# Optimization experiments

Measured on AMD Instinct MI355X. Metric: run time of the kernel, lower is better.

Reference implementation:

```python
import jax, jax.numpy as jnp
import numpy as np

B, H, V, W = 64, 4, 128000, 200  # batch, heads, vocab, repetition window
N = B * H
NEG = jnp.float32(-1e30)


def setup_inputs() -> dict:
    key = jax.random.key(0)
    ks = jax.random.split(key, 6)
    logits = jax.random.normal(ks[0], (B, H, V), jnp.float32) * 4.0
    output_tokens = jax.random.randint(ks[1], (N, W), 0, V)  # pad value would be V
    temperatures = jax.random.uniform(ks[2], (N,), jnp.float32, 0.5, 1.5)
    top_ps = jax.random.uniform(ks[3], (N,), jnp.float32, 0.7, 1.0)
    top_ks = jax.random.randint(ks[4], (N,), 1, 1025).astype(jnp.int32)
    repetition_penalties = jax.random.uniform(ks[5], (N,), jnp.float32, 1.0, 1.3)
    return {
        "logits": logits,
        "output_tokens": output_tokens,
        "temperatures": temperatures,
        "top_ps": top_ps,
        "top_ks": top_ks,
        "repetition_penalties": repetition_penalties,
    }


def reference(logits, output_tokens, temperatures, top_ps, top_ks, repetition_penalties):
    b, h, v = logits.shape
    n = b * h
    lg = logits.reshape(n, v)

    # --- repetition penalty (bincount-based mask, pad id = v is dropped) ---
    rows = jnp.arange(n)[:, None]
    counts = jnp.zeros((n, v + 1), jnp.int32).at[rows, output_tokens].add(1)[:, :v]
    seen = counts > 0
    rp = jnp.where(seen, repetition_penalties[:, None], 1.0)
    lg = jnp.where(lg > 0, lg / rp, lg * rp)

    # --- temperature ---
    lg = lg / temperatures[:, None]

    # --- top-k / top-p (vLLM: ascending sort, mask, scatter back) ---
    idx = jnp.argsort(lg, axis=-1)                       # ascending
    ls = jnp.take_along_axis(lg, idx, axis=-1)
    kth = jnp.take_along_axis(ls, (v - top_ks.astype(jnp.int32))[:, None], axis=-1)
    ls = jnp.where(ls < kth, NEG, ls)                    # top-k mask
    ps = jax.nn.softmax(ls, axis=-1)
    csum = jnp.cumsum(ps, axis=-1)
    pmask = (csum <= 1.0 - top_ps[:, None]).at[:, -1].set(False)
    ls = jnp.where(pmask, NEG, ls)                       # top-p mask
    inv = jnp.argsort(idx, axis=-1)                      # scatter back
    lg = jnp.take_along_axis(ls, inv, axis=-1)

    # --- softmax + multinomial sample (categorical == multinomial(probs, 1)) ---
    probs = jax.nn.softmax(lg, axis=-1)
    ids = jax.random.categorical(jax.random.key(42), lg, axis=-1).reshape(b, h)
    return ids, probs
```

## Files before the change

kernel.cpp:

```cpp
#include <hip/hip_runtime.h>

#define V 128000
#define V4 (V / 4)
#define NCHUNK (V / 16)
#define NROWS 256
#define NSLICE 8
#define SL4 (V4 / NSLICE)
#define W 200
#define VW (V / 32)
#define CAP 4096
#define CAPS 2048
#define CAPM 8192
#define TINYF 1.17549435e-38f
#define HIDX(b) ((b) + ((b) >> 5))
#define HSZ 4224

#define WS_CMAX   0u
#define WS_BMAX   4104192u
#define WS_NEED   16777216u

typedef float vfloat4 __attribute__((ext_vector_type(4)));

__device__ __forceinline__ unsigned int fkey(float x) {
  unsigned int u = __float_as_uint(x);
  return (u & 0x80000000u) ? ~u : (u | 0x80000000u);
}
__device__ __forceinline__ float ikey(unsigned int k) {
  unsigned int u = (k & 0x80000000u) ? (k & 0x7FFFFFFFu) : ~k;
  return __uint_as_float(u);
}

__device__ __forceinline__ unsigned int tf_bits(unsigned int t) {
  const unsigned int k0 = 0u, k1 = 42u;
  const unsigned int ks2 = k0 ^ k1 ^ 0x1BD11BDAu;
  unsigned int x0 = 0u + k0, x1 = t + k1;
  const unsigned int ksArr[3] = {k0, k1, ks2};
  const int RA[4] = {13, 15, 26, 6};
  const int RB[4] = {17, 29, 16, 24};
#pragma unroll
  for (int i = 0; i < 5; ++i) {
#pragma unroll
    for (int j = 0; j < 4; ++j) {
      int r = (i & 1) ? RB[j] : RA[j];
      x0 += x1;
      x1 = (x1 << r) | (x1 >> (32 - r));
      x1 ^= x0;
    }
    x0 += ksArr[(i + 1) % 3];
    x1 += ksArr[(i + 2) % 3] + (unsigned int)(i + 1);
  }
  return x0 ^ x1;
}

__device__ __forceinline__ float xform(float x, bool seen, float rp, float irp,
                                        float itemp) {
  if (seen) x = (x > 0.0f) ? x * irp : x * rp;
  return x * itemp;
}

__device__ __forceinline__ void wave_suffix_select_p(const int* hist, int need,
                                                     int lane, int* out_b,
                                                     int* out_rem) {
  int sm = 0;
  const int bb = lane * 64;
  for (int i = 0; i < 64; ++i) sm += hist[HIDX(bb + i)];
  int sfx = sm;
#pragma unroll
  for (int d = 1; d < 64; d <<= 1) {
    int t = __shfl_down(sfx, d);
    if (lane + d < 64) sfx += t;
  }
  unsigned long long mk = __ballot(sfx >= need);
  const int cstar = 63 - __builtin_clzll(mk);
  const int aboveC = __shfl(sfx, cstar) - __shfl(sm, cstar);
  int h = hist[HIDX(cstar * 64 + lane)];
  int sfx2 = h;
#pragma unroll
  for (int d = 1; d < 64; d <<= 1) {
    int t = __shfl_down(sfx2, d);
    if (lane + d < 64) sfx2 += t;
  }
  unsigned long long mk2 = __ballot(aboveC + sfx2 >= need);
  const int boff = 63 - __builtin_clzll(mk2);
  const int aboveB = aboveC + __shfl(sfx2, boff) - __shfl(h, boff);
  if (lane == 0) {
    *out_b = cstar * 64 + boff;
    *out_rem = need - aboveB;
  }
}

__global__ __launch_bounds__(256) void kAZ_chunkmax(
    const float* __restrict__ logits, const int* __restrict__ toks,
    const float* __restrict__ temps, const float* __restrict__ rps,
    unsigned short* __restrict__ ws_cmax, float* __restrict__ ws_bmax,
    float* __restrict__ probs) {
  __shared__ unsigned int s_seen[VW];
  __shared__ float s_red[4];
  const int row = blockIdx.x >> 3;
  const int slice = blockIdx.x & 7;
  const int tid = threadIdx.x;
  const int lane = tid & 63;
  const int wid = tid >> 6;
  const float rp = rps[row];
  const float irp = 1.0f / rp;
  const float itemp = 1.0f / temps[row];
  const size_t base = (size_t)row * V;
  const float4* __restrict__ lg4 = reinterpret_cast<const float4*>(logits + base);
  vfloat4* __restrict__ pr4 = reinterpret_cast<vfloat4*>(probs + base);

  for (int i = tid; i < VW; i += 256) s_seen[i] = 0u;
  __syncthreads();
  for (int i = tid; i < W; i += 256) {
    int tok = toks[row * W + i];
    if (tok >= 0 && tok < V) atomicOr(&s_seen[tok >> 5], 1u << (tok & 31));
  }
  __syncthreads();

  float lmax = -INFINITY;
  const int q0 = slice * SL4;
  const vfloat4 z4 = (vfloat4){0.0f, 0.0f, 0.0f, 0.0f};
  for (int qi = tid; qi < SL4; qi += 256) {
    const int q = q0 + qi;
    float4 x4 = lg4[q];
    pr4[q] = z4;
    float xs[4] = {x4.x, x4.y, x4.z, x4.w};
    const int j0 = q * 4;
    const int sh = j0 & 31;
    unsigned long long ww = (unsigned long long)s_seen[j0 >> 5] |
                            ((unsigned long long)s_seen[(j0 + 3) >> 5] << 32);
    unsigned int kmax = 0u;
#pragma unroll
    for (int e = 0; e < 4; ++e) {
      float x = xform(xs[e], (ww >> (sh + e)) & 1ull, rp, irp, itemp);
      lmax = fmaxf(lmax, x);
      unsigned int ky = fkey(x);
      kmax = kmax > ky ? kmax : ky;
    }
    unsigned int o;
    o = __shfl_xor(kmax, 1); kmax = kmax > o ? kmax : o;
    o = __shfl_xor(kmax, 2); kmax = kmax > o ? kmax : o;
    if ((lane & 3) == 0) ws_cmax[row * NCHUNK + (q >> 2)] = (unsigned short)(kmax >> 16);
  }
#pragma unroll
  for (int d = 32; d > 0; d >>= 1) lmax = fmaxf(lmax, __shfl_xor(lmax, d));
  if (lane == 0) s_red[wid] = lmax;
  __syncthreads();
  if (tid == 0) {
    float mm = fmaxf(fmaxf(s_red[0], s_red[1]), fmaxf(s_red[2], s_red[3]));
    ws_bmax[row * NSLICE + slice] = mm;
  }
}

__global__ __launch_bounds__(1024) void kB_select(
    const float* __restrict__ logits, const int* __restrict__ toks,
    const float* __restrict__ temps, const float* __restrict__ topps,
    const int* __restrict__ topks, const float* __restrict__ rps,
    const unsigned short* __restrict__ ws_cmax, const float* __restrict__ ws_bmax,
    float* __restrict__ out_ids, float* __restrict__ probs) {
  __shared__ unsigned long long s_key[CAP];
  __shared__ __align__(16) unsigned char s_bufA[HSZ*4];
  __shared__ __align__(16) unsigned char s_bufB[16384];
  __shared__ __align__(16) float s_e2[CAPS];
  __shared__ __align__(16) float s_q2[CAPS];
  __shared__ unsigned char s_keep[CAPS];
  __shared__ float s_wredf[16];
  __shared__ int s_wredi[16];
  __shared__ float s_mv, s_dn1, s_dn2;
  __shared__ int s_b0, s_cnt, s_scnt, s_selb, s_selrem, s_p0v, s_maxpop;

  int* s_hist0 = (int*)s_key;
  unsigned int* s_seen = (unsigned int*)s_bufA;
  int* s_hist = (int*)s_bufA;
  unsigned short* s_cmax16 = (unsigned short*)s_bufB;
  unsigned long long* s_key2 = (unsigned long long*)s_bufB;
  unsigned long long* s_skey = s_key;

  const int row = blockIdx.x;
  const int tid = threadIdx.x;
  const int lane = tid & 63;
  const int wid = tid >> 6;
  const float rp = rps[row];
  const float irp = 1.0f / rp;
  const float itemp = 1.0f / temps[row];
  const float topp = topps[row];
  const int k = topks[row];
  const size_t base = (size_t)row * V;
  const float4* __restrict__ lg4 = reinterpret_cast<const float4*>(logits + base);
  float* __restrict__ prow = probs + base;

  for (int i = tid; i < VW; i += 1024) s_seen[i] = 0u;
  for (int i = tid; i < HSZ; i += 1024) s_hist0[i] = 0;
  {
    const unsigned int* cm32 = reinterpret_cast<const unsigned int*>(ws_cmax + row * NCHUNK);
    unsigned int* sc32 = reinterpret_cast<unsigned int*>(s_cmax16);
    for (int i = tid; i < NCHUNK / 2; i += 1024) sc32[i] = cm32[i];
  }
  __syncthreads();
  for (int i = tid; i < W; i += 1024) {
    int tok = toks[row * W + i];
    if (tok >= 0 && tok < V) atomicOr(&s_seen[tok >> 5], 1u << (tok & 31));
  }
  for (int i = tid; i < NCHUNK; i += 1024)
    atomicAdd(&s_hist0[HIDX(s_cmax16[i] >> 4)], 1);
  __syncthreads();

  if (wid == 1 && lane == 0) {
    float mm = ws_bmax[row * NSLICE];
    for (int i = 1; i < NSLICE; ++i) mm = fmaxf(mm, ws_bmax[row * NSLICE + i]);
    s_mv = mm;
  }
  if (wid == 0) {
    wave_suffix_select_p(s_hist0, k, lane, &s_b0, &s_selrem);
    if (lane == 0) s_cnt = 0;
  }
  __syncthreads();
  const int b0 = s_b0;

  const unsigned int fk0 = ((unsigned int)b0) << 20;
  const int c16 = b0 << 4;
  for (int qb = 0; qb < V4; qb += 1024) {
    const int q = qb + tid;
    const bool act = (q < V4) && ((int)s_cmax16[q >> 2] >= c16);
    unsigned int ks[4];
    bool pr[4] = {false, false, false, false};
    const int j0 = q * 4;
    if (act) {
      float4 x4 = lg4[q];
      float raw[4] = {x4.x, x4.y, x4.z, x4.w};
      const int sh = j0 & 31;
      unsigned long long ww = (unsigned long long)s_seen[j0 >> 5] |
                              ((unsigned long long)s_seen[(j0 + 3) >> 5] << 32);
#pragma unroll
      for (int e = 0; e < 4; ++e) {
        float x = xform(raw[e], (ww >> (sh + e)) & 1ull, rp, irp, itemp);
        ks[e] = fkey(x);
        pr[e] = (ks[e] >= fk0);
      }
    }
    int cnt = (int)pr[0] + (int)pr[1] + (int)pr[2] + (int)pr[3];
    int inc = cnt;
#pragma unroll
    for (int d = 1; d < 64; d <<= 1) {
      int t = __shfl_up(inc, d);
      if (lane >= d) inc += t;
    }
    const int total = __shfl(inc, 63);
    if (total) {
      int basep = 0;
      if (lane == 0) basep = atomicAdd(&s_cnt, total);
      basep = __shfl(basep, 0);
      int off = basep + inc - cnt;
#pragma unroll
      for (int e = 0; e < 4; ++e) {
        if (pr[e]) {
          if (off < CAP)
            s_key[off] = ((unsigned long long)ks[e] << 32) | (unsigned int)(j0 + e);
          ++off;
        }
      }
    }
  }
  __syncthreads();
  int G = s_cnt;
  if (G > CAP) G = CAP;
  const int kk = k > G ? G : k;

  for (int i = tid; i < HSZ; i += 1024) s_hist[i] = 0;
  __syncthreads();
  for (int i = tid; i < G; i += 1024)
    atomicAdd(&s_hist[HIDX((unsigned int)(s_key[i] >> 52))], 1);
  __syncthreads();
  if (wid == 0) {
    wave_suffix_select_p(s_hist, kk, lane, &s_selb, &s_selrem);
    if (lane == 0) s_scnt = 0;
  }
  __syncthreads();
  const unsigned int b1 = (unsigned int)s_selb;

  for (int ib = 0; ib < G; ib += 1024) {
    const int i = ib + tid;
    const bool p = (i < G) && ((unsigned int)(s_key[i] >> 52) >= b1);
    unsigned long long mask = __ballot(p);
    if (!mask) continue;
    int basep = 0;
    if (lane == 0) basep = atomicAdd(&s_scnt, __popcll(mask));
    basep = __shfl(basep, 0);
    if (p) {
      int pos = basep + __popcll(mask & ((1ull << lane) - 1ull));
      if (pos < CAPS) s_key2[pos] = s_key[i];
    }
  }
  __syncthreads();
  int S = s_scnt;
  if (S > CAPS) S = CAPS;
  const float m = s_mv;

  const unsigned int cbase = b1 << 20;
  const unsigned int span = fkey(m) - cbase;
  int shiftb;
  {
    int bits = 32 - __clz((int)(span | 1u));
    shiftb = bits > 12 ? bits - 12 : 0;
  }
  for (int i = tid; i < HSZ; i += 1024) s_hist[i] = 0;
  __syncthreads();
  for (int i = tid; i < S; i += 1024) {
    unsigned int hi = (unsigned int)(s_key2[i] >> 32);
    int b = (int)((hi - cbase) >> shiftb);
    if (b > 4095) b = 4095;
    atomicAdd(&s_hist[HIDX(b)], 1);
  }
  __syncthreads();
  if (wid == 0) {
    int T = 0, mx = 0;
    const int bb = lane * 64;
    for (int i = 0; i < 64; ++i) {
      int c = s_hist[HIDX(bb + i)];
      T += c;
      mx = c > mx ? c : mx;
    }
    int ex = T;
#pragma unroll
    for (int d = 1; d < 64; d <<= 1) {
      int t = __shfl_up(ex, d);
      if (lane >= d) ex += t;
    }
    ex -= T;
    int run = ex;
    for (int i = 0; i < 64; ++i) {
      int idx = HIDX(bb + i);
      int c = s_hist[idx];
      s_hist[idx] = run;
      run += c;
    }
#pragma unroll
    for (int d = 32; d > 0; d >>= 1) {
      int o = __shfl_xor(mx, d);
      mx = o > mx ? o : mx;
    }
    if (lane == 0) s_maxpop = mx;
  }
  __syncthreads();

  if (s_maxpop <= 16) {
    for (int i = tid; i < S; i += 1024) {
      unsigned long long key = s_key2[i];
      unsigned int hi = (unsigned int)(key >> 32);
      int b = (int)((hi - cbase) >> shiftb);
      if (b > 4095) b = 4095;
      int pos = atomicAdd(&s_hist[HIDX(b)], 1);
      s_skey[pos] = key;
    }
    __syncthreads();
    for (int b = tid; b < 4096; b += 1024) {
      int endb = s_hist[HIDX(b)];
      int st = (b == 0) ? 0 : s_hist[HIDX(b - 1)];
      for (int i = st + 1; i < endb; ++i) {
        unsigned long long key = s_skey[i];
        int j = i - 1;
        while (j >= st && s_skey[j] > key) {
          s_skey[j + 1] = s_skey[j];
          --j;
        }
        s_skey[j + 1] = key;
      }
    }
    __syncthreads();
  } else {
    int np2 = 2;
    while (np2 < S) np2 <<= 1;
    for (int i = S + tid; i < np2; i += 1024) s_key2[i] = ~0ull;
    __syncthreads();
    for (int size = 2; size <= np2; size <<= 1) {
      for (int stride = size >> 1; stride > 0; stride >>= 1) {
        for (int t2 = tid; t2 < (np2 >> 1); t2 += 1024) {
          int pos = 2 * t2 - (t2 & (stride - 1));
          int qq = pos + stride;
          bool up = ((pos & size) == 0);
          unsigned long long a = s_key2[pos], b = s_key2[qq];
          if ((a > b) == up) { s_key2[pos] = b; s_key2[qq] = a; }
        }
        __syncthreads();
      }
    }
    for (int i = tid; i < S; i += 1024) s_skey[i] = s_key2[i];
    __syncthreads();
  }

  const unsigned int kthkey32 = (unsigned int)(s_skey[S - kk] >> 32);
  for (int i = tid; i < S; i += 1024) {
    unsigned int hi = (unsigned int)(s_skey[i] >> 32);
    if (hi >= kthkey32 && (i == 0 || (unsigned int)(s_skey[i - 1] >> 32) < kthkey32))
      s_p0v = i;
  }
  __syncthreads();
  const int p0 = s_p0v;
  const int L = S - p0;

  float part = 0.0f;
  for (int i = tid; i < L; i += 1024) {
    float x = ikey((unsigned int)(s_skey[p0 + i] >> 32));
    float e = expf(x - m);
    s_e2[i] = e;
    part += e;
  }
#pragma unroll
  for (int d = 32; d > 0; d >>= 1) part += __shfl_xor(part, d);
  if (lane == 0) s_wredf[wid] = part;
  __syncthreads();
  if (tid == 0) {
    float s = 0.0f;
    for (int i = 0; i < 16; ++i) s += s_wredf[i];
    s_dn1 = s;
  }
  __syncthreads();
  const float denom = s_dn1;

  for (int i = tid; i < L; i += 1024) s_q2[i] = s_e2[i] / denom;
  __syncthreads();

  if (tid == 0) {
    const float cut = 1.0f - topp;
    float cs = 0.0f;
    int i = 0;
    for (; i + 16 <= L; i += 16) {
      vfloat4 a = *(const vfloat4*)&s_q2[i];
      vfloat4 b = *(const vfloat4*)&s_q2[i + 4];
      vfloat4 c = *(const vfloat4*)&s_q2[i + 8];
      vfloat4 d = *(const vfloat4*)&s_q2[i + 12];
      unsigned int w0, w1, w2, w3;
      cs += a.x; w0  = (cs <= cut) ? 0u : 1u;
      cs += a.y; w0 |= ((cs <= cut) ? 0u : 1u) << 8;
      cs += a.z; w0 |= ((cs <= cut) ? 0u : 1u) << 16;
      cs += a.w; w0 |= ((cs <= cut) ? 0u : 1u) << 24;
      cs += b.x; w1  = (cs <= cut) ? 0u : 1u;
      cs += b.y; w1 |= ((cs <= cut) ? 0u : 1u) << 8;
      cs += b.z; w1 |= ((cs <= cut) ? 0u : 1u) << 16;
      cs += b.w; w1 |= ((cs <= cut) ? 0u : 1u) << 24;
      cs += c.x; w2  = (cs <= cut) ? 0u : 1u;
      cs += c.y; w2 |= ((cs <= cut) ? 0u : 1u) << 8;
      cs += c.z; w2 |= ((cs <= cut) ? 0u : 1u) << 16;
      cs += c.w; w2 |= ((cs <= cut) ? 0u : 1u) << 24;
      cs += d.x; w3  = (cs <= cut) ? 0u : 1u;
      cs += d.y; w3 |= ((cs <= cut) ? 0u : 1u) << 8;
      cs += d.z; w3 |= ((cs <= cut) ? 0u : 1u) << 16;
      cs += d.w; w3 |= ((cs <= cut) ? 0u : 1u) << 24;
      *(unsigned int*)&s_keep[i] = w0;
      *(unsigned int*)&s_keep[i + 4] = w1;
      *(unsigned int*)&s_keep[i + 8] = w2;
      *(unsigned int*)&s_keep[i + 12] = w3;
    }
    for (; i < L; ++i) {
      cs += s_q2[i];
      s_keep[i] = (cs <= cut) ? 0 : 1;
    }
    s_keep[L - 1] = 1;
  }
  __syncthreads();

  part = 0.0f;
  for (int i = tid; i < L; i += 1024)
    if (s_keep[i]) part += s_e2[i];
#pragma unroll
  for (int d = 32; d > 0; d >>= 1) part += __shfl_xor(part, d);
  if (lane == 0) s_wredf[wid] = part;
  __syncthreads();
  if (tid == 0) {
    float s = 0.0f;
    for (int i = 0; i < 16; ++i) s += s_wredf[i];
    s_dn2 = s;
  }
  __syncthreads();
  const float denom2 = s_dn2;

  for (int i = tid; i < L; i += 1024)
    s_e2[i] = s_keep[i] ? (s_e2[i] / denom2) : 0.0f;
  __syncthreads();

  float bs = -INFINITY;
  int bi = 0x7FFFFFFF;
  for (int i = tid; i < L; i += 1024) {
    if (!s_keep[i]) continue;
    unsigned long long kv = s_skey[p0 + i];
    int j = (int)(kv & 0xFFFFFFFFull);
    float x = ikey((unsigned int)(kv >> 32));
    unsigned int t = (unsigned int)(row * V) + (unsigned int)j;
    unsigned int bb = tf_bits(t);
    float u = __uint_as_float((bb >> 9) | 0x3f800000u) - 1.0f;
    if (u < TINYF) u = TINYF;
    float g = -logf(-logf(u));
    float sc = x + g;
    if (sc > bs || (sc == bs && j < bi)) { bs = sc; bi = j; }
  }

  for (int i = tid; i < L; i += 1024) {
    int j = (int)(s_skey[p0 + i] & 0xFFFFFFFFull);
    prow[j] = s_e2[i];
  }

#pragma unroll
  for (int d = 32; d > 0; d >>= 1) {
    float ov = __shfl_down(bs, d);
    int oi = __shfl_down(bi, d);
    if (ov > bs || (ov == bs && oi < bi)) { bs = ov; bi = oi; }
  }
  if (lane == 0) { s_wredf[wid] = bs; s_wredi[wid] = bi; }
  __syncthreads();
  if (tid == 0) {
    float bb = s_wredf[0];
    int bj = s_wredi[0];
    for (int i = 1; i < 16; ++i) {
      if (s_wredf[i] > bb || (s_wredf[i] == bb && s_wredi[i] < bj)) {
        bb = s_wredf[i];
        bj = s_wredi[i];
      }
    }
    out_ids[row] = (float)bj;
  }
}

__global__ __launch_bounds__(1024, 1) void sampler_mono(
    const float* __restrict__ logits, const int* __restrict__ toks,
    const float* __restrict__ temps, const float* __restrict__ topps,
    const int* __restrict__ topks, const float* __restrict__ rps,
    float* __restrict__ out_ids, float* __restrict__ probs) {
  __shared__ unsigned int s_seen[VW];
  __shared__ int s_hist[4096];
  __shared__ unsigned short s_cmax16[NCHUNK];
  __shared__ float s_sval[CAPM];
  __shared__ int s_sidx[CAPM];
  __shared__ float s_e[CAPM];
  __shared__ unsigned char s_keep[CAPM];
  __shared__ float s_wredf[16];
  __shared__ int s_wredi[16];
  __shared__ float s_m, s_denom, s_denom2;
  __shared__ int s_b0, s_cnt, s_p0;

  const int row = blockIdx.x;
  const int tid = threadIdx.x;
  const int lane = tid & 63;
  const int wid = tid >> 6;
  const float rp = rps[row];
  const float irp = 1.0f / rp;
  const float itemp = 1.0f / temps[row];
  const float topp = topps[row];
  const int k = topks[row];
  const size_t base = (size_t)row * V;
  const float4* __restrict__ lg4 = reinterpret_cast<const float4*>(logits + base);
  vfloat4* __restrict__ pr4 = reinterpret_cast<vfloat4*>(probs + base);

  for (int i = tid; i < VW; i += 1024) s_seen[i] = 0u;
  for (int i = tid; i < 4096; i += 1024) s_hist[i] = 0;
  __syncthreads();
  for (int i = tid; i < W; i += 1024) {
    int tok = toks[row * W + i];
    if (tok >= 0 && tok < V) atomicOr(&s_seen[tok >> 5], 1u << (tok & 31));
  }
  __syncthreads();

  float lmax = -INFINITY;
  for (int qb = 0; qb < V4; qb += 1024) {
    const int q = qb + tid;
    unsigned int kmax = 0u;
    if (q < V4) {
      float4 x4 = lg4[q];
      float xs[4] = {x4.x, x4.y, x4.z, x4.w};
      const int j0 = q * 4;
      const int sh = j0 & 31;
      unsigned long long ww = (unsigned long long)s_seen[j0 >> 5] |
                              ((unsigned long long)s_seen[(j0 + 3) >> 5] << 32);
#pragma unroll
      for (int e = 0; e < 4; ++e) {
        float x = xform(xs[e], (ww >> (sh + e)) & 1ull, rp, irp, itemp);
        lmax = fmaxf(lmax, x);
        unsigned int ky = fkey(x);
        kmax = kmax > ky ? kmax : ky;
      }
    }
    unsigned int o;
    o = __shfl_xor(kmax, 1); kmax = kmax > o ? kmax : o;
    o = __shfl_xor(kmax, 2); kmax = kmax > o ? kmax : o;
    if (((lane & 3) == 0) && (q < V4)) s_cmax16[q >> 2] = (unsigned short)(kmax >> 16);
  }
#pragma unroll
  for (int d = 32; d > 0; d >>= 1) lmax = fmaxf(lmax, __shfl_xor(lmax, d));
  if (lane == 0) s_wredf[wid] = lmax;
  __syncthreads();
  for (int i = tid; i < NCHUNK; i += 1024)
    atomicAdd(&s_hist[s_cmax16[i] >> 4], 1);
  __syncthreads();
  if (wid == 1 && lane == 0) {
    float mm = s_wredf[0];
    for (int i = 1; i < 16; ++i) mm = fmaxf(mm, s_wredf[i]);
    s_m = mm;
  }
  if (wid == 0) {
    int sm = 0;
    const int bb = lane * 64;
    for (int i = 0; i < 64; ++i) sm += s_hist[bb + i];
    int sfx = sm;
#pragma unroll
    for (int d = 1; d < 64; d <<= 1) {
      int t = __shfl_down(sfx, d);
      if (lane + d < 64) sfx += t;
    }
    unsigned long long mk = __ballot(sfx >= k);
    const int cstar = 63 - __builtin_clzll(mk);
    const int above = __shfl(sfx, cstar) - __shfl(sm, cstar);
    int h = s_hist[cstar * 64 + lane];
    int sfx2 = h;
#pragma unroll
    for (int d = 1; d < 64; d <<= 1) {
      int t = __shfl_down(sfx2, d);
      if (lane + d < 64) sfx2 += t;
    }
    unsigned long long mk2 = __ballot(above + sfx2 >= k);
    const int boff = 63 - __builtin_clzll(mk2);
    if (lane == 0) { s_b0 = cstar * 64 + boff; s_cnt = 0; }
  }
  __syncthreads();
  const int b0 = s_b0;
  const unsigned int fk0 = ((unsigned int)b0) << 20;
  const int c16 = b0 << 4;
  for (int qb = 0; qb < V4; qb += 1024) {
    const int q = qb + tid;
    const bool act = (q < V4) && ((int)s_cmax16[q >> 2] >= c16);
    float xs[4];
    bool pr[4] = {false, false, false, false};
    const int j0 = q * 4;
    if (act) {
      float4 x4 = lg4[q];
      float raw[4] = {x4.x, x4.y, x4.z, x4.w};
      const int sh = j0 & 31;
      unsigned long long ww = (unsigned long long)s_seen[j0 >> 5] |
                              ((unsigned long long)s_seen[(j0 + 3) >> 5] << 32);
#pragma unroll
      for (int e = 0; e < 4; ++e) {
        xs[e] = xform(raw[e], (ww >> (sh + e)) & 1ull, rp, irp, itemp);
        pr[e] = (fkey(xs[e]) >= fk0);
      }
    }
#pragma unroll
    for (int e = 0; e < 4; ++e) {
      unsigned long long mask = __ballot(pr[e]);
      if (!mask) continue;
      int basep = 0;
      if (lane == 0) basep = atomicAdd(&s_cnt, __popcll(mask));
      basep = __shfl(basep, 0);
      if (pr[e]) {
        int pos = basep + __popcll(mask & ((1ull << lane) - 1ull));
        if (pos < CAPM) { s_sval[pos] = xs[e]; s_sidx[pos] = j0 + e; }
      }
    }
  }
  __syncthreads();
  int G = s_cnt;
  if (G > CAPM) G = CAPM;
  int np2 = 2;
  while (np2 < G) np2 <<= 1;
  for (int i = G + tid; i < np2; i += 1024) {
    s_sval[i] = INFINITY;
    s_sidx[i] = 0x7FFFFFFF;
  }
  __syncthreads();
  for (int size = 2; size <= np2; size <<= 1) {
    for (int stride = size >> 1; stride > 0; stride >>= 1) {
      for (int t2 = tid; t2 < (np2 >> 1); t2 += 1024) {
        int pos = 2 * t2 - (t2 & (stride - 1));
        int qq = pos + stride;
        bool up = ((pos & size) == 0);
        float v1 = s_sval[pos], v2 = s_sval[qq];
        int i1 = s_sidx[pos], i2 = s_sidx[qq];
        bool gt = (v1 > v2) || (v1 == v2 && i1 > i2);
        if (gt == up) {
          s_sval[pos] = v2; s_sval[qq] = v1;
          s_sidx[pos] = i2; s_sidx[qq] = i1;
        }
      }
      __syncthreads();
    }
  }
  const int kk = k > G ? G : k;
  const float kth = s_sval[G - kk];
  const float m = s_m;
  for (int i = tid; i < G; i += 1024) {
    if (s_sval[i] >= kth && (i == 0 || s_sval[i - 1] < kth)) s_p0 = i;
  }
  __syncthreads();
  const int p0 = s_p0;
  float part = 0.0f;
  for (int i = p0 + tid; i < G; i += 1024) {
    float e = expf(s_sval[i] - m);
    s_e[i] = e;
    part += e;
  }
#pragma unroll
  for (int d = 32; d > 0; d >>= 1) part += __shfl_xor(part, d);
  if (lane == 0) s_wredf[wid] = part;
  __syncthreads();
  if (tid == 0) {
    float s = 0.0f;
    for (int i = 0; i < 16; ++i) s += s_wredf[i];
    s_denom = s;
  }
  __syncthreads();
  const float denom = s_denom;
  if (tid == 0) {
    const float cut = 1.0f - topp;
    float cs = 0.0f;
    for (int i = p0; i < G; ++i) {
      cs += s_e[i] / denom;
      s_keep[i] = (cs <= cut) ? 0 : 1;
    }
    s_keep[G - 1] = 1;
  }
  __syncthreads();
  part = 0.0f;
  for (int i = p0 + tid; i < G; i += 1024)
    if (s_keep[i]) part += s_e[i];
#pragma unroll
  for (int d = 32; d > 0; d >>= 1) part += __shfl_xor(part, d);
  if (lane == 0) s_wredf[wid] = part;
  __syncthreads();
  if (tid == 0) {
    float s = 0.0f;
    for (int i = 0; i < 16; ++i) s += s_wredf[i];
    s_denom2 = s;
  }
  __syncthreads();
  const float denom2 = s_denom2;
  for (int i = p0 + tid; i < G; i += 1024)
    s_e[i] = s_keep[i] ? (s_e[i] / denom2) : 0.0f;
  __syncthreads();
  float bs = -INFINITY;
  int bi = 0x7FFFFFFF;
  for (int i = p0 + tid; i < G; i += 1024) {
    if (!s_keep[i]) continue;
    int j = s_sidx[i];
    unsigned int t = (unsigned int)(row * V) + (unsigned int)j;
    unsigned int bb = tf_bits(t);
    float u = __uint_as_float((bb >> 9) | 0x3f800000u) - 1.0f;
    if (u < TINYF) u = TINYF;
    float g = -logf(-logf(u));
    float sc = s_sval[i] + g;
    if (sc > bs || (sc == bs && j < bi)) { bs = sc; bi = j; }
  }
  const unsigned int kkey = fkey(kth);
  const int k16 = (int)(kkey >> 16);
  for (int q = tid; q < V4; q += 1024) {
    vfloat4 o = (vfloat4){0.0f, 0.0f, 0.0f, 0.0f};
    if ((int)s_cmax16[q >> 2] >= k16) {
      float4 x4 = lg4[q];
      float raw[4] = {x4.x, x4.y, x4.z, x4.w};
      float os[4];
      const int j0 = q * 4;
      const int sh = j0 & 31;
      unsigned long long ww = (unsigned long long)s_seen[j0 >> 5] |
                              ((unsigned long long)s_seen[(j0 + 3) >> 5] << 32);
#pragma unroll
      for (int e = 0; e < 4; ++e) {
        float x = xform(raw[e], (ww >> (sh + e)) & 1ull, rp, irp, itemp);
        float pr = 0.0f;
        if (x >= kth) {
          int j = j0 + e;
          int lo = p0, hi = G;
          while (lo < hi) {
            int mid = (lo + hi) >> 1;
            float v = s_sval[mid];
            int id = s_sidx[mid];
            if (v < x || (v == x && id < j)) lo = mid + 1; else hi = mid;
          }
          pr = s_e[lo];
        }
        os[e] = pr;
      }
      o.x = os[0]; o.y = os[1]; o.z = os[2]; o.w = os[3];
    }
    pr4[q] = o;
  }
#pragma unroll
  for (int d = 32; d > 0; d >>= 1) {
    float ov = __shfl_down(bs, d);
    int oi = __shfl_down(bi, d);
    if (ov > bs || (ov == bs && oi < bi)) { bs = ov; bi = oi; }
  }
  if (lane == 0) { s_wredf[wid] = bs; s_wredi[wid] = bi; }
  __syncthreads();
  if (tid == 0) {
    float bb = s_wredf[0];
    int bj = s_wredi[0];
    for (int i = 1; i < 16; ++i) {
      if (s_wredf[i] > bb || (s_wredf[i] == bb && s_wredi[i] < bj)) {
        bb = s_wredf[i];
        bj = s_wredi[i];
      }
    }
    out_ids[row] = (float)bj;
  }
}

extern "C" void kernel_launch(void* const* d_in, const int* in_sizes, int n_in,
                              void* d_out, int out_size, void* d_ws, size_t ws_size,
                              hipStream_t stream) {
  (void)in_sizes; (void)out_size;
  if (n_in < 6) return;
  const float* logits = (const float*)d_in[0];
  const int* toks = (const int*)d_in[1];
  const float* temps = (const float*)d_in[2];
  const float* topps = (const float*)d_in[3];
  const int* topks = (const int*)d_in[4];
  const float* rps = (const float*)d_in[5];
  float* out = (float*)d_out;
  float* probs = out + NROWS;

  if (ws_size >= WS_NEED && d_ws != nullptr) {
    char* w = (char*)d_ws;
    unsigned short* ws_cmax = (unsigned short*)(w + WS_CMAX);
    float* ws_bmax = (float*)(w + WS_BMAX);
    kAZ_chunkmax<<<dim3(NROWS * NSLICE), dim3(256), 0, stream>>>(
        logits, toks, temps, rps, ws_cmax, ws_bmax, probs);
    kB_select<<<dim3(NROWS), dim3(1024), 0, stream>>>(
        logits, toks, temps, topps, topks, rps, ws_cmax, ws_bmax, out, probs);
  } else {
    sampler_mono<<<dim3(NROWS), dim3(1024), 0, stream>>>(
        logits, toks, temps, topps, topks, rps, out, probs);
  }
}
```

Measured before the change: 119.9 us.

## Move probs zeroing into select kernel and use LDS-only barriers

Zero-filling of the probs output moves from the chunk-max kernel into the select kernel's candidate scan loop, so the first kernel only reads logits. Block barriers in the select kernel are replaced by a barrier that waits only on LDS counters, so outstanding global zero-stores do not stall each barrier. This aims to overlap the large output write with the selection work. It risks lower store bandwidth with only one block per row, and the later scattered writes to probs may not be ordered after the zero stores from other threads.

Result: faster. 100.6 us (-16.1%).

```diff
diff --git a/kernel.cpp b/kernel.cpp
--- a/kernel.cpp
+++ b/kernel.cpp
@@ -21,6 +21,11 @@
 
 typedef float vfloat4 __attribute__((ext_vector_type(4)));
 
+__device__ __forceinline__ void bar_lds() {
+  asm volatile("s_waitcnt lgkmcnt(0)" ::: "memory");
+  __builtin_amdgcn_s_barrier();
+}
+
 __device__ __forceinline__ unsigned int fkey(float x) {
   unsigned int u = __float_as_uint(x);
   return (u & 0x80000000u) ? ~u : (u | 0x80000000u);
@@ -89,11 +94,10 @@
   }
 }
 
-__global__ __launch_bounds__(256) void kAZ_chunkmax(
+__global__ __launch_bounds__(256) void kA_chunkmax(
     const float* __restrict__ logits, const int* __restrict__ toks,
     const float* __restrict__ temps, const float* __restrict__ rps,
-    unsigned short* __restrict__ ws_cmax, float* __restrict__ ws_bmax,
-    float* __restrict__ probs) {
+    unsigned short* __restrict__ ws_cmax, float* __restrict__ ws_bmax) {
   __shared__ unsigned int s_seen[VW];
   __shared__ float s_red[4];
   const int row = blockIdx.x >> 3;
@@ -106,7 +110,6 @@
   const float itemp = 1.0f / temps[row];
   const size_t base = (size_t)row * V;
   const float4* __restrict__ lg4 = reinterpret_cast<const float4*>(logits + base);
-  vfloat4* __restrict__ pr4 = reinterpret_cast<vfloat4*>(probs + base);
 
   for (int i = tid; i < VW; i += 256) s_seen[i] = 0u;
   __syncthreads();
@@ -118,11 +121,9 @@
 
   float lmax = -INFINITY;
   const int q0 = slice * SL4;
-  const vfloat4 z4 = (vfloat4){0.0f, 0.0f, 0.0f, 0.0f};
   for (int qi = tid; qi < SL4; qi += 256) {
     const int q = q0 + qi;
     float4 x4 = lg4[q];
-    pr4[q] = z4;
     float xs[4] = {x4.x, x4.y, x4.z, x4.w};
     const int j0 = q * 4;
     const int sh = j0 & 31;
@@ -187,6 +188,7 @@
   const size_t base = (size_t)row * V;
   const float4* __restrict__ lg4 = reinterpret_cast<const float4*>(logits + base);
   float* __restrict__ prow = probs + base;
+  vfloat4* __restrict__ pr4 = reinterpret_cast<vfloat4*>(prow);
 
   for (int i = tid; i < VW; i += 1024) s_seen[i] = 0u;
   for (int i = tid; i < HSZ; i += 1024) s_hist0[i] = 0;
@@ -216,10 +218,12 @@
   __syncthreads();
   const int b0 = s_b0;
 
+  const vfloat4 z4 = (vfloat4){0.0f, 0.0f, 0.0f, 0.0f};
   const unsigned int fk0 = ((unsigned int)b0) << 20;
   const int c16 = b0 << 4;
   for (int qb = 0; qb < V4; qb += 1024) {
     const int q = qb + tid;
+    if (q < V4) pr4[q] = z4;
     const bool act = (q < V4) && ((int)s_cmax16[q >> 2] >= c16);
     unsigned int ks[4];
     bool pr[4] = {false, false, false, false};
@@ -260,21 +264,21 @@
       }
     }
   }
-  __syncthreads();
+  bar_lds();
   int G = s_cnt;
   if (G > CAP) G = CAP;
   const int kk = k > G ? G : k;
 
   for (int i = tid; i < HSZ; i += 1024) s_hist[i] = 0;
-  __syncthreads();
+  bar_lds();
   for (int i = tid; i < G; i += 1024)
     atomicAdd(&s_hist[HIDX((unsigned int)(s_key[i] >> 52))], 1);
-  __syncthreads();
+  bar_lds();
   if (wid == 0) {
     wave_suffix_select_p(s_hist, kk, lane, &s_selb, &s_selrem);
     if (lane == 0) s_scnt = 0;
   }
-  __syncthreads();
+  bar_lds();
   const unsigned int b1 = (unsigned int)s_selb;
 
   for (int ib = 0; ib < G; ib += 1024) {
@@ -290,7 +294,7 @@
       if (pos < CAPS) s_key2[pos] = s_key[i];
     }
   }
-  __syncthreads();
+  bar_lds();
   int S = s_scnt;
   if (S > CAPS) S = CAPS;
   const float m = s_mv;
@@ -303,14 +307,14 @@
     shiftb = bits > 12 ? bits - 12 : 0;
   }
   for (int i = tid; i < HSZ; i += 1024) s_hist[i] = 0;
-  __syncthreads();
+  bar_lds();
   for (int i = tid; i < S; i += 1024) {
     unsigned int hi = (unsigned int)(s_key2[i] >> 32);
     int b = (int)((hi - cbase) >> shiftb);
     if (b > 4095) b = 4095;
     atomicAdd(&s_hist[HIDX(b)], 1);
   }
-  __syncthreads();
+  bar_lds();
   if (wid == 0) {
     int T = 0, mx = 0;
     const int bb = lane * 64;
@@ -340,7 +344,7 @@
     }
     if (lane == 0) s_maxpop = mx;
   }
-  __syncthreads();
+  bar_lds();
 
   if (s_maxpop <= 16) {
     for (int i = tid; i < S; i += 1024) {
@@ -351,7 +355,7 @@
       int pos = atomicAdd(&s_hist[HIDX(b)], 1);
       s_skey[pos] = key;
     }
-    __syncthreads();
+    bar_lds();
     for (int b = tid; b < 4096; b += 1024) {
       int endb = s_hist[HIDX(b)];
       int st = (b == 0) ? 0 : s_hist[HIDX(b - 1)];
@@ -365,12 +369,12 @@
         s_skey[j + 1] = key;
       }
     }
-    __syncthreads();
+    bar_lds();
   } else {
     int np2 = 2;
     while (np2 < S) np2 <<= 1;
     for (int i = S + tid; i < np2; i += 1024) s_key2[i] = ~0ull;
-    __syncthreads();
+    bar_lds();
     for (int size = 2; size <= np2; size <<= 1) {
       for (int stride = size >> 1; stride > 0; stride >>= 1) {
         for (int t2 = tid; t2 < (np2 >> 1); t2 += 1024) {
@@ -380,11 +384,11 @@
           unsigned long long a = s_key2[pos], b = s_key2[qq];
           if ((a > b) == up) { s_key2[pos] = b; s_key2[qq] = a; }
         }
-        __syncthreads();
+        bar_lds();
       }
     }
     for (int i = tid; i < S; i += 1024) s_skey[i] = s_key2[i];
-    __syncthreads();
+    bar_lds();
   }
 
   const unsigned int kthkey32 = (unsigned int)(s_skey[S - kk] >> 32);
@@ -393,7 +397,7 @@
     if (hi >= kthkey32 && (i == 0 || (unsigned int)(s_skey[i - 1] >> 32) < kthkey32))
       s_p0v = i;
   }
-  __syncthreads();
+  bar_lds();
   const int p0 = s_p0v;
   const int L = S - p0;
 
@@ -407,17 +411,17 @@
 #pragma unroll
   for (int d = 32; d > 0; d >>= 1) part += __shfl_xor(part, d);
   if (lane == 0) s_wredf[wid] = part;
-  __syncthreads();
+  bar_lds();
   if (tid == 0) {
     float s = 0.0f;
     for (int i = 0; i < 16; ++i) s += s_wredf[i];
     s_dn1 = s;
   }
-  __syncthreads();
+  bar_lds();
   const float denom = s_dn1;
 
   for (int i = tid; i < L; i += 1024) s_q2[i] = s_e2[i] / denom;
-  __syncthreads();
+  bar_lds();
 
   if (tid == 0) {
     const float cut = 1.0f - topp;
@@ -456,7 +460,7 @@
     }
     s_keep[L - 1] = 1;
   }
-  __syncthreads();
+  bar_lds();
 
   part = 0.0f;
   for (int i = tid; i < L; i += 1024)
@@ -464,13 +468,13 @@
 #pragma unroll
   for (int d = 32; d > 0; d >>= 1) part += __shfl_xor(part, d);
   if (lane == 0) s_wredf[wid] = part;
-  __syncthreads();
+  bar_lds();
   if (tid == 0) {
     float s = 0.0f;
     for (int i = 0; i < 16; ++i) s += s_wredf[i];
     s_dn2 = s;
   }
-  __syncthreads();
+  bar_lds();
   const float denom2 = s_dn2;
 
   for (int i = tid; i < L; i += 1024)
@@ -505,7 +509,7 @@
     if (ov > bs || (ov == bs && oi < bi)) { bs = ov; bi = oi; }
   }
   if (lane == 0) { s_wredf[wid] = bs; s_wredi[wid] = bi; }
-  __syncthreads();
+  bar_lds();
   if (tid == 0) {
     float bb = s_wredf[0];
     int bj = s_wredi[0];
@@ -817,8 +821,8 @@
     char* w = (char*)d_ws;
     unsigned short* ws_cmax = (unsigned short*)(w + WS_CMAX);
     float* ws_bmax = (float*)(w + WS_BMAX);
-    kAZ_chunkmax<<<dim3(NROWS * NSLICE), dim3(256), 0, stream>>>(
-        logits, toks, temps, rps, ws_cmax, ws_bmax, probs);
+    kA_chunkmax<<<dim3(NROWS * NSLICE), dim3(256), 0, stream>>>(
+        logits, toks, temps, rps, ws_cmax, ws_bmax);
     kB_select<<<dim3(NROWS), dim3(1024), 0, stream>>>(
         logits, toks, temps, topps, topks, rps, ws_cmax, ws_bmax, out, probs);
   } else {
```
